# Performance work log

Hardware: AMD Instinct MI355X
Metric: run time of the kernel (lower is better)

Reference implementation:

```python
import jax, jax.numpy as jnp
import numpy as np

N_NODES = 100000
N_EDGES = 1600000
N_GRAPHS = 512
HID = 192
EPS = 1e-5


def setup_inputs() -> dict:
    key = jax.random.key(0)
    ks = jax.random.split(key, 16)
    x = jax.random.normal(ks[0], (N_NODES, 1), dtype=jnp.float32)
    edge_index = jax.random.randint(ks[1], (2, N_EDGES), 0, N_NODES, dtype=jnp.int64)
    batch = jnp.sort(jax.random.randint(ks[2], (N_NODES,), 0, N_GRAPHS, dtype=jnp.int64))
    def lin(k, fi, fo):
        # torch nn.Linear default init: U(-1/sqrt(fi), 1/sqrt(fi))
        b = 1.0 / np.sqrt(fi)
        return jax.random.uniform(k, (fi, fo), jnp.float32, -b, b)
    return {
        "x": x, "edge_index": edge_index, "batch": batch,
        "W1": lin(ks[3], 1, HID), "b1": jnp.zeros((HID,), jnp.float32),
        "g1": jnp.ones((HID,), jnp.float32), "be1": jnp.zeros((HID,), jnp.float32), "a1": jnp.ones((HID,), jnp.float32),
        "W2": lin(ks[4], HID, HID), "b2": jnp.zeros((HID,), jnp.float32),
        "g2": jnp.ones((HID,), jnp.float32), "be2": jnp.zeros((HID,), jnp.float32), "a2": jnp.ones((HID,), jnp.float32),
        "Wc1": lin(ks[5], HID, HID // 2), "bc1": jax.random.uniform(ks[6], (HID // 2,), jnp.float32, -1/np.sqrt(HID), 1/np.sqrt(HID)),
        "Wc2": lin(ks[7], HID // 2, 4), "bc2": jax.random.uniform(ks[8], (4,), jnp.float32, -1/np.sqrt(HID // 2), 1/np.sqrt(HID // 2)),
    }


def gcn_conv(x, W, b, row, col, n):
    # PyG GCNConv: h = xW; add self-loops; norm = d^-1/2[src] * d^-1/2[dst]; scatter-add to dst; + bias
    h = x @ W
    sl = jnp.arange(n, dtype=row.dtype)
    r = jnp.concatenate([row, sl])
    c = jnp.concatenate([col, sl])
    deg = jax.ops.segment_sum(jnp.ones_like(c, dtype=h.dtype), c, num_segments=n)
    dinv = jnp.where(deg > 0, jax.lax.rsqrt(deg), 0.0)
    norm = dinv[r] * dinv[c]                      # [E+N]
    msg = h[r] * norm[:, None]                    # [E+N, HID] dominant gather
    return jax.ops.segment_sum(msg, c, num_segments=n) + b


def graph_norm(x, batch, gamma, beta, alpha, g):
    cnt = jax.ops.segment_sum(jnp.ones((x.shape[0],), x.dtype), batch, num_segments=g)
    cnt = jnp.maximum(cnt, 1.0)[:, None]
    mean = jax.ops.segment_sum(x, batch, num_segments=g) / cnt
    out = x - alpha * mean[batch]
    var = jax.ops.segment_sum(out * out, batch, num_segments=g) / cnt
    out = out * jax.lax.rsqrt(var + EPS)[batch]
    return gamma * out + beta


def reference(x, edge_index, batch, W1, b1, g1, be1, a1, W2, b2, g2, be2, a2, Wc1, bc1, Wc2, bc2):
    n = x.shape[0]
    row, col = edge_index[0], edge_index[1]
    h = gcn_conv(x, W1, b1, row, col, n)
    h = jax.nn.relu(graph_norm(h, batch, g1, be1, a1, N_GRAPHS))
    h = gcn_conv(h, W2, b2, row, col, n)
    h = jax.nn.relu(graph_norm(h, batch, g2, be2, a2, N_GRAPHS))
    # global mean pool (dropout is identity in eval mode)
    cnt = jnp.maximum(jax.ops.segment_sum(jnp.ones((n,), h.dtype), batch, num_segments=N_GRAPHS), 1.0)
    pooled = jax.ops.segment_sum(h, batch, num_segments=N_GRAPHS) / cnt[:, None]
    z = jax.nn.relu(pooled @ Wc1 + bc1)
    return z @ Wc2 + bc2
```

## Files before the change

### kernel.cpp

```cpp
#include <hip/hip_runtime.h>
#include <hip/hip_bf16.h>
#include <hip/hip_fp16.h>

#define N_NODES 100000
#define N_PAD 100032
#define N_EDGES 1600000
#define N_GRAPHS 512
#define HID 192
#define EPSV 1e-5f

using f16x8 = __attribute__((ext_vector_type(8))) _Float16;
using f16x4 = __attribute__((ext_vector_type(4))) _Float16;
using f32x4 = __attribute__((ext_vector_type(4))) float;

__global__ void k_count(const int* __restrict__ col, int* __restrict__ cnt) {
    int e = blockIdx.x * blockDim.x + threadIdx.x;
    if (e < N_EDGES) atomicAdd(&cnt[col[e]], 1);
}

__global__ void k_misc(const float* __restrict__ W2, _Float16* __restrict__ W2h,
                       const int* __restrict__ batch, int* __restrict__ gstart) {
    int id = blockIdx.x * blockDim.x + threadIdx.x;
    if (id < HID * HID) W2h[id] = (_Float16)W2[id];
    int g = id - HID * HID;
    if (g >= 0 && g <= N_GRAPHS) {
        if (g == N_GRAPHS) { gstart[g] = N_NODES; return; }
        int lo = 0, hi = N_NODES;
        while (lo < hi) { int mid = (lo + hi) >> 1; if (batch[mid] < g) lo = mid + 1; else hi = mid; }
        gstart[g] = lo;
    }
}

__global__ void k_scan_partial(const int* __restrict__ cnt, int* __restrict__ bsum) {
    __shared__ int sd[256];
    int base = blockIdx.x * 1024;
    int t = threadIdx.x;
    int s = 0;
    for (int j = 0; j < 4; ++j) {
        int i = base + j * 256 + t;
        if (i < N_NODES) s += cnt[i];
    }
    sd[t] = s; __syncthreads();
    for (int off = 128; off > 0; off >>= 1) {
        if (t < off) sd[t] += sd[t + off];
        __syncthreads();
    }
    if (t == 0) bsum[blockIdx.x] = sd[0];
}

__global__ void k_scan_final(const int* __restrict__ cnt, const int* __restrict__ bsum,
                             int nb, int* __restrict__ row_ptr, int* __restrict__ cursor,
                             float* __restrict__ dinv, const float* __restrict__ x,
                             float* __restrict__ xp) {
    __shared__ int sd[256];
    __shared__ int s_off;
    int bid = blockIdx.x;
    int t = threadIdx.x;
    int part = 0;
    for (int i = t; i < bid; i += 256) part += bsum[i];
    sd[t] = part; __syncthreads();
    for (int off = 128; off > 0; off >>= 1) {
        if (t < off) sd[t] += sd[t + off];
        __syncthreads();
    }
    if (t == 0) s_off = sd[0];
    __syncthreads();
    int base = bid * 1024;
    int idx0 = base + t * 4;
    int c[4]; int tot = 0;
    for (int j = 0; j < 4; ++j) {
        int i = idx0 + j;
        c[j] = (i < N_NODES) ? cnt[i] : 0;
        tot += c[j];
    }
    sd[t] = tot; __syncthreads();
    for (int off = 1; off < 256; off <<= 1) {
        int v = (t >= off) ? sd[t - off] : 0;
        __syncthreads();
        sd[t] += v;
        __syncthreads();
    }
    int excl = sd[t] - tot + s_off;
    for (int j = 0; j < 4; ++j) {
        int i = idx0 + j;
        if (i < N_NODES) {
            row_ptr[i] = excl;
            cursor[i] = excl;
            float dv = rsqrtf((float)(c[j] + 1));
            dinv[i] = dv;
            xp[i] = x[i] * dv;
            excl += c[j];
        }
    }
    if (bid == nb - 1 && t == 255) row_ptr[N_NODES] = excl;
}

#define FILL_PASSES 8
#define FILL_RANGE (N_NODES / FILL_PASSES)
__global__ void __launch_bounds__(256) k_fill(const int* __restrict__ row,
                                              const int* __restrict__ col,
                                              int* __restrict__ cursor,
                                              int* __restrict__ csr_src,
                                              int* __restrict__ csr_off) {
    int tid = blockIdx.x * blockDim.x + threadIdx.x;
    int stride = gridDim.x * blockDim.x;
    for (int p = 0; p < FILL_PASSES; ++p) {
        int lo = p * FILL_RANGE;
        int hi = (p == FILL_PASSES - 1) ? N_NODES : lo + FILL_RANGE;
        for (int e = tid; e < N_EDGES; e += stride) {
            int c = col[e];
            if (c >= lo && c < hi) {
                int r = row[e];
                int pos = atomicAdd(&cursor[c], 1);
                csr_src[pos] = r;
                csr_off[pos] = r * (HID * 2);
            }
        }
    }
}

__global__ void k_layer1(const float* __restrict__ x, const float* __restrict__ xp,
                         const int* __restrict__ batch,
                         const int* __restrict__ row_ptr, const int* __restrict__ csr_src,
                         const float* __restrict__ dinv, float4* __restrict__ node_info) {
    int v = blockIdx.x * blockDim.x + threadIdx.x;
    if (v >= N_NODES) return;
    int e0 = row_ptr[v], e1 = row_ptr[v + 1];
    float acc = 0.f;
    for (int base = e0; base < e1; base += 16) {
        int src[16]; float xv[16];
#pragma unroll
        for (int j = 0; j < 16; ++j) { int e = base + j; src[j] = csr_src[(e < e1) ? e : e0]; }
#pragma unroll
        for (int j = 0; j < 16; ++j) { xv[j] = xp[src[j]]; }
#pragma unroll
        for (int j = 0; j < 16; ++j) { acc += (base + j < e1) ? xv[j] : 0.f; }
    }
    float dv = dinv[v];
    float u = dv * acc + x[v] * dv * dv;
    node_info[v] = make_float4(u, dv, __int_as_float((int)batch[v]), 0.f);
}

__global__ void __launch_bounds__(192) k_stats_ab(const float4* __restrict__ node_info,
                                                  const int* __restrict__ gstart,
                                                  const float* __restrict__ W1, const float* __restrict__ b1,
                                                  const float* __restrict__ g1, const float* __restrict__ be1,
                                                  const float* __restrict__ a1,
                                                  float* __restrict__ A, float* __restrict__ B) {
    __shared__ float sd[192], sd2[192];
    int g = blockIdx.x, t = threadIdx.x;
    int i0 = gstart[g], i1 = gstart[g + 1];
    float s = 0.f, s2 = 0.f;
    for (int i = i0 + t; i < i1; i += 192) { float u = node_info[i].x; s += u; s2 += u * u; }
    sd[t] = s; sd2[t] = s2; __syncthreads();
    for (int off = 96; off >= 3; off >>= 1) {
        if (t < off) { sd[t] += sd[t + off]; sd2[t] += sd2[t + off]; }
        __syncthreads();
    }
    float sum_u = sd[0] + sd[1] + sd[2];
    float sum_u2 = sd2[0] + sd2[1] + sd2[2];
    float cntf = fmaxf((float)(i1 - i0), 1.f);
    float m = sum_u / cntf;
    float es2 = sum_u2 / cntf;
    int f = t;
    float w = W1[f], bb = b1[f], al = a1[f];
    float c2 = bb * (1.f - al);
    float d = al * m;
    float eud2 = es2 - 2.f * d * m + d * d;
    float var = w * w * eud2 + 2.f * w * c2 * (m - d) + c2 * c2;
    float rs = rsqrtf(var + EPSV);
    float gam = g1[f];
    A[g * HID + f] = gam * rs * w;
    B[g * HID + f] = gam * rs * (c2 - w * d) + be1[f];
}

__global__ void __launch_bounds__(256) k_x1(const float4* __restrict__ node_info,
                                            const float* __restrict__ A,
                                            const float* __restrict__ B,
                                            _Float16* __restrict__ X1p) {
    int wid = threadIdx.x >> 6;
    int lane = threadIdx.x & 63;
    int v = blockIdx.x * 4 + wid;
    if (v >= N_NODES) return;
    float4 ni = node_info[v];
    float u = ni.x, dv = ni.y;
    int g = __float_as_int(ni.z);
    int c4 = (lane < 48 ? lane : 47) * 4;
    float4 Av = *(const float4*)(A + g * HID + c4);
    float4 Bv = *(const float4*)(B + g * HID + c4);
    f16x4 o;
    o[0] = (_Float16)(fmaxf(fmaf(Av.x, u, Bv.x), 0.f) * dv);
    o[1] = (_Float16)(fmaxf(fmaf(Av.y, u, Bv.y), 0.f) * dv);
    o[2] = (_Float16)(fmaxf(fmaf(Av.z, u, Bv.z), 0.f) * dv);
    o[3] = (_Float16)(fmaxf(fmaf(Av.w, u, Bv.w), 0.f) * dv);
    if (lane < 48) *(f16x4*)(X1p + (size_t)v * HID + c4) = o;
}

#define CH 8
__global__ void __launch_bounds__(256) k_conv2(const _Float16* __restrict__ X1p,
                                               const float* __restrict__ dinv,
                                               const int* __restrict__ row_ptr,
                                               const int* __restrict__ csr_off,
                                               _Float16* __restrict__ aggh) {
    int wid = threadIdx.x >> 6;
    int lane = threadIdx.x & 63;
    int v = blockIdx.x * 4 + wid;
    if (v >= N_NODES) return;
    unsigned c8 = (unsigned)(lane < 48 ? lane : 47) * 8u;
    const char* Xb = (const char*)X1p;
    float dv = dinv[v];
    f16x4 sv = *(const f16x4*)(Xb + (unsigned)v * (HID * 2) + c8);
    float a0 = (float)sv[0], a1 = (float)sv[1], a2 = (float)sv[2], a3 = (float)sv[3];
    int e0 = row_ptr[v], e1 = row_ptr[v + 1];
    for (int b = e0; b < e1; b += CH) {
        unsigned off[CH]; float wgt[CH];
#pragma unroll
        for (int j = 0; j < CH; ++j) {
            int e = b + j;
            off[j] = (unsigned)csr_off[(e < e1) ? e : e0] + c8;
            wgt[j] = (e < e1) ? 1.f : 0.f;
        }
        f16x4 rv[CH];
#pragma unroll
        for (int j = 0; j < CH; ++j)
            rv[j] = *(const f16x4*)(Xb + off[j]);
#pragma unroll
        for (int j = 0; j < CH; ++j) {
            a0 = fmaf(wgt[j], (float)rv[j][0], a0);
            a1 = fmaf(wgt[j], (float)rv[j][1], a1);
            a2 = fmaf(wgt[j], (float)rv[j][2], a2);
            a3 = fmaf(wgt[j], (float)rv[j][3], a3);
        }
    }
    if (lane < 48) {
        f16x4 o;
        o[0] = (_Float16)(a0 * dv);
        o[1] = (_Float16)(a1 * dv);
        o[2] = (_Float16)(a2 * dv);
        o[3] = (_Float16)(a3 * dv);
        *(f16x4*)((char*)aggh + (unsigned)v * (HID * 2) + c8) = o;
    }
}

#define BM 64
__global__ void __launch_bounds__(256) k_gemm(const _Float16* __restrict__ A,
                                              const _Float16* __restrict__ W,
                                              const float* __restrict__ b2,
                                              _Float16* __restrict__ H) {
    __shared__ _Float16 a_lds[BM * HID];
    int t = threadIdx.x;
    int wid = t >> 6, lane = t & 63;
    int row0 = blockIdx.x * BM;
    const char* Ablk = (const char*)(A + (size_t)row0 * HID);
#pragma unroll
    for (int it = 0; it < 6; ++it) {
        int bo = (it * 256 + t) * 16;
        int r = bo / 384;
        int swz = bo ^ ((r & 7) << 4);
        *(float4*)((char*)a_lds + swz) = *(const float4*)(Ablk + bo);
    }
    int n0 = wid * 48;
    int bn = n0 + (lane & 15);
    int bk0 = (lane >> 4) << 3;
    f16x8 bfr[6][3];
#pragma unroll
    for (int kc = 0; kc < 6; ++kc)
#pragma unroll
        for (int nt = 0; nt < 3; ++nt) {
            const _Float16* src = W + (size_t)(kc * 32 + bk0) * HID + bn + nt * 16;
            f16x8 v;
#pragma unroll
            for (int j = 0; j < 8; ++j) v[j] = src[(size_t)j * HID];
            bfr[kc][nt] = v;
        }
    __syncthreads();
    f32x4 acc[4][3];
#pragma unroll
    for (int mt = 0; mt < 4; ++mt)
#pragma unroll
        for (int nt = 0; nt < 3; ++nt) acc[mt][nt] = (f32x4){0.f, 0.f, 0.f, 0.f};
    int ar = lane & 15;
#pragma unroll
    for (int mt = 0; mt < 4; ++mt) {
        int r = mt * 16 + ar;
        int rbase = r * 384;
        int sw = (r & 7) << 4;
#pragma unroll
        for (int kc = 0; kc < 6; ++kc) {
            int bo = (rbase + (kc * 32 + bk0) * 2) ^ sw;
            f16x8 a = *(const f16x8*)((const char*)a_lds + bo);
            acc[mt][0] = __builtin_amdgcn_mfma_f32_16x16x32_f16(a, bfr[kc][0], acc[mt][0], 0, 0, 0);
            acc[mt][1] = __builtin_amdgcn_mfma_f32_16x16x32_f16(a, bfr[kc][1], acc[mt][1], 0, 0, 0);
            acc[mt][2] = __builtin_amdgcn_mfma_f32_16x16x32_f16(a, bfr[kc][2], acc[mt][2], 0, 0, 0);
        }
    }
    int cn = lane & 15;
    int rb = (lane >> 4) * 4;
    float bias[3];
#pragma unroll
    for (int nt = 0; nt < 3; ++nt) bias[nt] = b2[n0 + nt * 16 + cn];
#pragma unroll
    for (int mt = 0; mt < 4; ++mt)
#pragma unroll
        for (int nt = 0; nt < 3; ++nt) {
            int col = n0 + nt * 16 + cn;
#pragma unroll
            for (int r = 0; r < 4; ++r) {
                int grow = row0 + mt * 16 + rb + r;
                if (grow < N_NODES)
                    H[(size_t)grow * HID + col] = (_Float16)(acc[mt][nt][r] + bias[nt]);
            }
        }
}

__global__ void __launch_bounds__(192) k_stats2(const _Float16* __restrict__ h,
                                                const int* __restrict__ batch,
                                                float* __restrict__ sums,
                                                float* __restrict__ sumsq) {
    int f = threadIdx.x;
    int r0 = blockIdx.x * 64;
    int r1 = min(r0 + 64, N_NODES);
    int g = batch[r0];
    float s = 0.f, s2 = 0.f;
    int i = r0;
    for (; i + 4 <= r1; i += 4) {
        int g0 = batch[i], g3 = batch[i + 3];
        float v0 = (float)h[(size_t)(i + 0) * HID + f];
        float v1 = (float)h[(size_t)(i + 1) * HID + f];
        float v2 = (float)h[(size_t)(i + 2) * HID + f];
        float v3 = (float)h[(size_t)(i + 3) * HID + f];
        if (g0 == g && g3 == g) {
            s += v0 + v1 + v2; s += v3;
            s2 += v0 * v0 + v1 * v1; s2 += v2 * v2 + v3 * v3;
        } else {
            float vv[4] = {v0, v1, v2, v3};
            for (int j = 0; j < 4; ++j) {
                int gi = batch[i + j];
                if (gi != g) {
                    atomicAdd(&sums[g * HID + f], s);
                    atomicAdd(&sumsq[g * HID + f], s2);
                    s = 0.f; s2 = 0.f; g = gi;
                }
                s += vv[j]; s2 += vv[j] * vv[j];
            }
        }
    }
    for (; i < r1; ++i) {
        int gi = batch[i];
        float v = (float)h[(size_t)i * HID + f];
        if (gi != g) {
            atomicAdd(&sums[g * HID + f], s);
            atomicAdd(&sumsq[g * HID + f], s2);
            s = 0.f; s2 = 0.f; g = gi;
        }
        s += v; s2 += v * v;
    }
    atomicAdd(&sums[g * HID + f], s);
    atomicAdd(&sumsq[g * HID + f], s2);
}

__global__ void k_cd(const float* __restrict__ sums, const float* __restrict__ sumsq,
                     const int* __restrict__ gstart,
                     const float* __restrict__ g2, const float* __restrict__ be2,
                     const float* __restrict__ a2,
                     float* __restrict__ C, float* __restrict__ D) {
    int id = blockIdx.x * blockDim.x + threadIdx.x;
    if (id >= N_GRAPHS * HID) return;
    int g = id / HID, f = id % HID;
    float cntf = fmaxf((float)(gstart[g + 1] - gstart[g]), 1.f);
    float mh = sums[id] / cntf;
    float msq = sumsq[id] / cntf;
    float al = a2[f];
    float var = msq - 2.f * al * mh * mh + al * al * mh * mh;
    float Cv = g2[f] * rsqrtf(var + EPSV);
    C[id] = Cv;
    D[id] = be2[f] - Cv * al * mh;
}

__global__ void __launch_bounds__(192) k_pool(const _Float16* __restrict__ h,
                                              const int* __restrict__ batch,
                                              const float* __restrict__ C,
                                              const float* __restrict__ D,
                                              float* __restrict__ pooled) {
    int f = threadIdx.x;
    int r0 = blockIdx.x * 64;
    int r1 = min(r0 + 64, N_NODES);
    int g = batch[r0];
    float Cg = C[g * HID + f], Dg = D[g * HID + f];
    float s = 0.f;
    int i = r0;
    for (; i + 4 <= r1; i += 4) {
        int g0 = batch[i], g3 = batch[i + 3];
        float v0 = (float)h[(size_t)(i + 0) * HID + f];
        float v1 = (float)h[(size_t)(i + 1) * HID + f];
        float v2 = (float)h[(size_t)(i + 2) * HID + f];
        float v3 = (float)h[(size_t)(i + 3) * HID + f];
        if (g0 == g && g3 == g) {
            s += fmaxf(fmaf(Cg, v0, Dg), 0.f) + fmaxf(fmaf(Cg, v1, Dg), 0.f);
            s += fmaxf(fmaf(Cg, v2, Dg), 0.f) + fmaxf(fmaf(Cg, v3, Dg), 0.f);
        } else {
            float vv[4] = {v0, v1, v2, v3};
            for (int j = 0; j < 4; ++j) {
                int gi = batch[i + j];
                if (gi != g) {
                    atomicAdd(&pooled[g * HID + f], s);
                    s = 0.f; g = gi;
                    Cg = C[g * HID + f]; Dg = D[g * HID + f];
                }
                s += fmaxf(fmaf(Cg, vv[j], Dg), 0.f);
            }
        }
    }
    for (; i < r1; ++i) {
        int gi = batch[i];
        float v = (float)h[(size_t)i * HID + f];
        if (gi != g) {
            atomicAdd(&pooled[g * HID + f], s);
            s = 0.f; g = gi;
            Cg = C[g * HID + f]; Dg = D[g * HID + f];
        }
        s += fmaxf(fmaf(Cg, v, Dg), 0.f);
    }
    atomicAdd(&pooled[g * HID + f], s);
}

__global__ void __launch_bounds__(128) k_mlp(const float* __restrict__ pooled,
                                             const int* __restrict__ gstart,
                                             const float* __restrict__ Wc1,
                                             const float* __restrict__ bc1,
                                             const float* __restrict__ Wc2,
                                             const float* __restrict__ bc2,
                                             float* __restrict__ out) {
    __shared__ float p[HID];
    __shared__ float z[96];
    int g = blockIdx.x, t = threadIdx.x;
    float inv = 1.f / fmaxf((float)(gstart[g + 1] - gstart[g]), 1.f);
    for (int i = t; i < HID; i += 128) p[i] = pooled[g * HID + i] * inv;
    __syncthreads();
    if (t < 96) {
        float acc = bc1[t];
        for (int k = 0; k < HID; ++k) acc += p[k] * Wc1[k * 96 + t];
        z[t] = fmaxf(acc, 0.f);
    }
    __syncthreads();
    if (t < 4) {
        float acc = bc2[t];
        for (int j = 0; j < 96; ++j) acc += z[j] * Wc2[j * 4 + t];
        out[g * 4 + t] = acc;
    }
}

extern "C" void kernel_launch(void* const* d_in, const int* in_sizes, int n_in,
                              void* d_out, int out_size, void* d_ws, size_t ws_size,
                              hipStream_t stream) {
    const float* x   = (const float*)d_in[0];
    const int* eidx  = (const int*)d_in[1];
    const int* batch = (const int*)d_in[2];
    const float* W1  = (const float*)d_in[3];
    const float* b1  = (const float*)d_in[4];
    const float* g1  = (const float*)d_in[5];
    const float* be1 = (const float*)d_in[6];
    const float* a1  = (const float*)d_in[7];
    const float* W2  = (const float*)d_in[8];
    const float* b2  = (const float*)d_in[9];
    const float* g2  = (const float*)d_in[10];
    const float* be2 = (const float*)d_in[11];
    const float* a2  = (const float*)d_in[12];
    const float* Wc1 = (const float*)d_in[13];
    const float* bc1 = (const float*)d_in[14];
    const float* Wc2 = (const float*)d_in[15];
    const float* bc2 = (const float*)d_in[16];
    const int* row = eidx;
    const int* col = eidx + N_EDGES;
    float* out = (float*)d_out;

    char* ws = (char*)d_ws;
    size_t off = 0;
    auto alloc = [&](size_t bytes) -> char* {
        char* p = ws + off;
        off = (off + bytes + 255) & ~(size_t)255;
        return p;
    };
    int*   cnt     = (int*)  alloc(N_NODES * 4);
    float* sums2   = (float*)alloc(N_GRAPHS * HID * 4);
    float* sumsq2  = (float*)alloc(N_GRAPHS * HID * 4);
    float* pooled  = (float*)alloc(N_GRAPHS * HID * 4);
    size_t zbytes  = off;
    int*   bsum    = (int*)  alloc(128 * 4);
    int*   row_ptr = (int*)  alloc((N_NODES + 1) * 4);
    int*   cursor  = (int*)  alloc(N_NODES * 4);
    int*   csr_src = (int*)  alloc(N_EDGES * 4);
    int*   csr_off = (int*)  alloc(N_EDGES * 4);
    float* dinv    = (float*)alloc(N_NODES * 4);
    float* xp      = (float*)alloc(N_NODES * 4);
    float4* node_info = (float4*)alloc((size_t)N_NODES * 16);
    float* Atab    = (float*)alloc(N_GRAPHS * HID * 4);
    float* Btab    = (float*)alloc(N_GRAPHS * HID * 4);
    float* Ctab    = (float*)alloc(N_GRAPHS * HID * 4);
    float* Dtab    = (float*)alloc(N_GRAPHS * HID * 4);
    int*   gstart  = (int*)  alloc((N_GRAPHS + 1) * 4);
    _Float16* X1p  = (_Float16*)alloc((size_t)N_NODES * HID * 2);
    _Float16* aggh = (_Float16*)alloc((size_t)N_PAD * HID * 2);
    _Float16* h2   = (_Float16*)alloc((size_t)N_NODES * HID * 2);
    _Float16* W2h  = (_Float16*)alloc((size_t)HID * HID * 2);

    hipMemsetAsync(ws, 0, zbytes, stream);
    k_misc<<<(HID * HID + N_GRAPHS + 1 + 255) / 256, 256, 0, stream>>>(W2, W2h, batch, gstart);
    k_count<<<(N_EDGES + 255) / 256, 256, 0, stream>>>(col, cnt);
    int PB = (N_NODES + 1023) / 1024;
    k_scan_partial<<<PB, 256, 0, stream>>>(cnt, bsum);
    k_scan_final<<<PB, 256, 0, stream>>>(cnt, bsum, PB, row_ptr, cursor, dinv, x, xp);
    k_fill<<<2048, 256, 0, stream>>>(row, col, cursor, csr_src, csr_off);
    k_layer1<<<(N_NODES + 255) / 256, 256, 0, stream>>>(x, xp, batch, row_ptr, csr_src, dinv, node_info);
    k_stats_ab<<<N_GRAPHS, 192, 0, stream>>>(node_info, gstart, W1, b1, g1, be1, a1, Atab, Btab);
    k_x1<<<(N_NODES + 3) / 4, 256, 0, stream>>>(node_info, Atab, Btab, X1p);
    k_conv2<<<(N_NODES + 3) / 4, 256, 0, stream>>>(X1p, dinv, row_ptr, csr_off, aggh);
    k_gemm<<<(N_NODES + BM - 1) / BM, 256, 0, stream>>>(aggh, W2h, b2, h2);
    int SB = (N_NODES + 63) / 64;
    k_stats2<<<SB, 192, 0, stream>>>(h2, batch, sums2, sumsq2);
    k_cd<<<(N_GRAPHS * HID + 255) / 256, 256, 0, stream>>>(sums2, sumsq2, gstart,
                                                           g2, be2, a2, Ctab, Dtab);
    k_pool<<<SB, 192, 0, stream>>>(h2, batch, Ctab, Dtab, pooled);
    k_mlp<<<N_GRAPHS, 128, 0, stream>>>(pooled, gstart, Wc1, bc1, Wc2, bc2, out);
}
```

Baseline: 372.1 us.

## Restructure CSR fill into concurrent destination windows and drop csr_off array

The CSR fill kernel no longer sweeps every edge eight times in sequential passes. Each block now owns one destination-range window (blockIdx & 7) and one contiguous edge chunk, so the eight windows run concurrently and each edge is read by eight blocks instead of every thread reading it eight times. The precomputed byte-offset array csr_off is removed, and conv2 computes the offset from csr_src with a multiply, which saves a 6.4 MB write and the allocation. Atomics into each cursor region are now spread over time rather than grouped by window, which may reduce the locality the original pass ordering aimed for.

```diff
diff --git a/kernel.cpp b/kernel.cpp
--- a/kernel.cpp
+++ b/kernel.cpp
@@ -95,26 +95,24 @@
     if (bid == nb - 1 && t == 255) row_ptr[N_NODES] = excl;
 }
 
-#define FILL_PASSES 8
-#define FILL_RANGE (N_NODES / FILL_PASSES)
+#define FILL_WIN 8
+#define FILL_RANGE (N_NODES / FILL_WIN)
+#define EPR ((N_EDGES + 255) / 256)
 __global__ void __launch_bounds__(256) k_fill(const int* __restrict__ row,
                                               const int* __restrict__ col,
                                               int* __restrict__ cursor,
-                                              int* __restrict__ csr_src,
-                                              int* __restrict__ csr_off) {
-    int tid = blockIdx.x * blockDim.x + threadIdx.x;
-    int stride = gridDim.x * blockDim.x;
-    for (int p = 0; p < FILL_PASSES; ++p) {
-        int lo = p * FILL_RANGE;
-        int hi = (p == FILL_PASSES - 1) ? N_NODES : lo + FILL_RANGE;
-        for (int e = tid; e < N_EDGES; e += stride) {
-            int c = col[e];
-            if (c >= lo && c < hi) {
-                int r = row[e];
-                int pos = atomicAdd(&cursor[c], 1);
-                csr_src[pos] = r;
-                csr_off[pos] = r * (HID * 2);
-            }
+                                              int* __restrict__ csr_src) {
+    int w = blockIdx.x & 7;
+    int rank = blockIdx.x >> 3;
+    int lo = w * FILL_RANGE;
+    int hi = (w == FILL_WIN - 1) ? N_NODES : lo + FILL_RANGE;
+    int e0 = rank * EPR;
+    int e1 = min(e0 + EPR, N_EDGES);
+    for (int e = e0 + threadIdx.x; e < e1; e += 256) {
+        int c = col[e];
+        if (c >= lo && c < hi) {
+            int pos = atomicAdd(&cursor[c], 1);
+            csr_src[pos] = row[e];
         }
     }
 }
@@ -200,7 +198,7 @@
 __global__ void __launch_bounds__(256) k_conv2(const _Float16* __restrict__ X1p,
                                                const float* __restrict__ dinv,
                                                const int* __restrict__ row_ptr,
-                                               const int* __restrict__ csr_off,
+                                               const int* __restrict__ csr_src,
                                                _Float16* __restrict__ aggh) {
     int wid = threadIdx.x >> 6;
     int lane = threadIdx.x & 63;
@@ -217,7 +215,7 @@
 #pragma unroll
         for (int j = 0; j < CH; ++j) {
             int e = b + j;
-            off[j] = (unsigned)csr_off[(e < e1) ? e : e0] + c8;
+            off[j] = (unsigned)csr_src[(e < e1) ? e : e0] * (unsigned)(HID * 2) + c8;
             wgt[j] = (e < e1) ? 1.f : 0.f;
         }
         f16x4 rv[CH];
@@ -490,7 +488,6 @@
     int*   row_ptr = (int*)  alloc((N_NODES + 1) * 4);
     int*   cursor  = (int*)  alloc(N_NODES * 4);
     int*   csr_src = (int*)  alloc(N_EDGES * 4);
-    int*   csr_off = (int*)  alloc(N_EDGES * 4);
     float* dinv    = (float*)alloc(N_NODES * 4);
     float* xp      = (float*)alloc(N_NODES * 4);
     float4* node_info = (float4*)alloc((size_t)N_NODES * 16);
@@ -510,11 +507,11 @@
     int PB = (N_NODES + 1023) / 1024;
     k_scan_partial<<<PB, 256, 0, stream>>>(cnt, bsum);
     k_scan_final<<<PB, 256, 0, stream>>>(cnt, bsum, PB, row_ptr, cursor, dinv, x, xp);
-    k_fill<<<2048, 256, 0, stream>>>(row, col, cursor, csr_src, csr_off);
+    k_fill<<<2048, 256, 0, stream>>>(row, col, cursor, csr_src);
     k_layer1<<<(N_NODES + 255) / 256, 256, 0, stream>>>(x, xp, batch, row_ptr, csr_src, dinv, node_info);
     k_stats_ab<<<N_GRAPHS, 192, 0, stream>>>(node_info, gstart, W1, b1, g1, be1, a1, Atab, Btab);
     k_x1<<<(N_NODES + 3) / 4, 256, 0, stream>>>(node_info, Atab, Btab, X1p);
-    k_conv2<<<(N_NODES + 3) / 4, 256, 0, stream>>>(X1p, dinv, row_ptr, csr_off, aggh);
+    k_conv2<<<(N_NODES + 3) / 4, 256, 0, stream>>>(X1p, dinv, row_ptr, csr_src, aggh);
     k_gemm<<<(N_NODES + BM - 1) / BM, 256, 0, stream>>>(aggh, W2h, b2, h2);
     int SB = (N_NODES + 63) / 64;
     k_stats2<<<SB, 192, 0, stream>>>(h2, batch, sums2, sumsq2);
```

Measured after the change: 348.0 us. 1.07x faster.
